# Optimization experiments

Hardware: AMD Instinct MI355X
Metric: run time of the kernel (lower is better)

## Reference

```python
import jax, jax.numpy as jnp
import numpy as np
from jax import lax

B, H, W, Q, C = 2, 96, 96, 30000, 64
DIMS = [C * 9 + 4, 256, 256, 256, 256, 3]  # imnet MLP


def setup_inputs() -> dict:
    key = jax.random.key(0)
    ks = jax.random.split(key, 20)
    d = {}
    d["inp"] = jax.random.normal(ks[0], (B, 3, H, W), jnp.float32)
    d["coord"] = jax.random.uniform(ks[1], (B, Q, 2), jnp.float32) * 2.0 - 1.0
    d["cell"] = jax.random.uniform(ks[2], (B, Q, 2), jnp.float32) * (2.0 / 256.0)
    d["conv_w"] = jax.random.normal(ks[3], (C, 3, 3, 3), jnp.float32) * 0.1
    d["conv_b"] = jnp.zeros((C,), jnp.float32)
    for i in range(5):
        fan_in = DIMS[i]
        d[f"w{i}"] = jax.random.normal(ks[4 + i], (DIMS[i], DIMS[i + 1]), jnp.float32) / np.sqrt(fan_in)
        d[f"b{i}"] = jnp.zeros((DIMS[i + 1],), jnp.float32)
    return d


def _liif_forward(inp, coord, cell, conv_w, conv_b, ws, bs):
    # encoder: 3x3 conv + tanh (gen_feat)
    feat = lax.conv_general_dilated(inp, conv_w, (1, 1), "SAME",
                                    dimension_numbers=("NCHW", "OIHW", "NCHW"))
    feat = jnp.tanh(feat + conv_b[None, :, None, None])  # [B,C,H,W]
    b, c, h, w = feat.shape

    # feat_unfold: F.unfold(feat, 3, padding=1) -> [B, C*9, H, W]
    pad = jnp.pad(feat, ((0, 0), (0, 0), (1, 1), (1, 1)))
    patches = jnp.stack([pad[:, :, i:i + h, j:j + w] for i in range(3) for j in range(3)], axis=2)
    fu = patches.reshape(b, c * 9, h, w).transpose(0, 2, 3, 1)  # [B,H,W,9C]

    # local ensemble offsets
    offsets = jnp.array([[-1., -1.], [-1., 1.], [1., -1.], [1., 1.]], jnp.float32)
    rad = jnp.array([1.0 / h, 1.0 / w], jnp.float32)  # 2/r/2
    eps = 1e-6
    ec = coord[None] + (offsets * rad)[:, None, None, :] + eps  # [4,B,Q,2]
    ec = jnp.clip(ec, -1 + 1e-10, 1 - 1e-10)

    # grid_sample nearest, align_corners=False: ix = ((x+1)*size - 1)/2, round
    iy = jnp.clip(jnp.round((ec[..., 0] + 1) * h / 2 - 0.5).astype(jnp.int32), 0, h - 1)
    ix = jnp.clip(jnp.round((ec[..., 1] + 1) * w / 2 - 0.5).astype(jnp.int32), 0, w - 1)
    b_idx = jnp.arange(b)[None, :, None]  # [1,B,1]
    q_feat = fu[b_idx, iy, ix]  # [4,B,Q,9C]

    # feat_coord (make_coord): pixel-center coords in [-1,1]
    yc = (-1.0 + (2.0 * jnp.arange(h, dtype=jnp.float32) + 1.0) / h)
    xc = (-1.0 + (2.0 * jnp.arange(w, dtype=jnp.float32) + 1.0) / w)
    fc = jnp.stack(jnp.meshgrid(yc, xc, indexing="ij"), axis=-1)  # [H,W,2]
    q_coord = fc[iy, ix]  # [4,B,Q,2]

    scale = jnp.array([h, w], jnp.float32)
    rel_coord = (coord[None] - q_coord) * scale  # [4,B,Q,2]
    rel_cell = cell * scale  # [B,Q,2]

    x = jnp.concatenate(
        [q_feat, rel_coord, jnp.broadcast_to(rel_cell[None], rel_coord.shape)], axis=-1)  # [4,B,Q,580]

    # imnet MLP
    for wi, bi in zip(ws[:-1], bs[:-1]):
        x = jax.nn.relu(x @ wi + bi)
    x = x @ ws[-1] + bs[-1]  # [4,B,Q,3]

    areas = jnp.abs(jnp.prod(rel_coord, axis=-1, keepdims=True)) + 1e-9
    areas = areas / jnp.sum(areas, axis=0, keepdims=True)
    areas = areas[::-1]  # swap diagonal ensemble weights

    out = jnp.sum(x * areas, axis=0)  # [B,Q,3]
    return jnp.tanh(out) * 1.01  # fat_tanh(eps=0.01)


def reference(inp, coord, cell, conv_w, conv_b, w0, b0, w1, b1, w2, b2, w3, b3, w4, b4):
    return _liif_forward(inp, coord, cell, conv_w, conv_b,
                         [w0, w1, w2, w3, w4], [b0, b1, b2, b3, b4])
```

## Files before the change

kernel.cpp:

```cpp
#include <hip/hip_runtime.h>


typedef _Float16 half8   __attribute__((ext_vector_type(8)));
typedef _Float16 half4v  __attribute__((ext_vector_type(4)));
typedef _Float16 half2v  __attribute__((ext_vector_type(2)));
typedef float    float4v __attribute__((ext_vector_type(4)));
typedef float    floatx16 __attribute__((ext_vector_type(16)));

__device__ __forceinline__ _Float16 to_h(float v) {
  return (_Float16)fminf(fmaxf(v, -60000.0f), 60000.0f);
}

#define NQ 30000
#define QT 469
#define QTP 472

__global__ void prep_kernel(const float* __restrict__ w0,
                            const float* __restrict__ w1,
                            const float* __restrict__ w2,
                            const float* __restrict__ w3,
                            const float* __restrict__ w4,
                            _Float16* __restrict__ p0, _Float16* __restrict__ p1,
                            _Float16* __restrict__ p2, _Float16* __restrict__ p3,
                            _Float16* __restrict__ p4) {
  int idx = blockIdx.x * 256 + threadIdx.x;
  if (idx < 151552) {
    int kb = idx >> 11, rem = idx & 2047;
    int n = rem >> 3, i = rem & 7;
    int f = kb * 8 + i;
    float v = 0.0f;
    if (f < 576)      v = w0[((f & 63) * 9 + (f >> 6)) * 256 + n];
    else if (f < 580) v = w0[f * 256 + n];
    p0[idx] = (_Float16)v;
  } else if (idx < 348160) {
    int j = idx - 151552;
    int l = j >> 16;
    int j2 = j & 65535;
    int kb = j2 >> 11, rem = j2 & 2047;
    int n = rem >> 3, i = rem & 7;
    int k = kb * 8 + i;
    const float* w = (l == 0) ? w1 : (l == 1) ? w2 : w3;
    _Float16* p = (l == 0) ? p1 : (l == 1) ? p2 : p3;
    p[j2] = (_Float16)w[k * 256 + n];
  } else if (idx < 352256) {
    int j = idx - 348160;
    int kb = j >> 7, rem = j & 127;
    int n = rem >> 3, i = rem & 7;
    int k = kb * 8 + i;
    float v = (n < 3) ? w4[k * 3 + n] : 0.0f;
    p4[j] = (_Float16)v;
  }
}

__global__ void conv_kernel(const float* __restrict__ inp,
                            const float* __restrict__ cw,
                            const float* __restrict__ cb,
                            _Float16* __restrict__ P) {
  __shared__ __align__(16) float s_w[1728];
  __shared__ __align__(16) float s_b[64];
  for (int i = threadIdx.x; i < 1728; i += 256) s_w[i] = cw[i];
  if (threadIdx.x < 64) s_b[threadIdx.x] = cb[threadIdx.x];
  __syncthreads();
  int tid = blockIdx.x * 256 + threadIdx.x;
  if (tid >= 2 * 98 * 98) return;
  int b = tid / 9604;
  int rem = tid % 9604;
  int yy = rem / 98, xx = rem % 98;
  alignas(16) _Float16 outv[64];
  if (yy == 0 || yy == 97 || xx == 0 || xx == 97) {
#pragma unroll
    for (int c = 0; c < 64; ++c) outv[c] = (_Float16)0.0f;
  } else {
    int y = yy - 1, x = xx - 1;
    float win[27];
#pragma unroll
    for (int ci = 0; ci < 3; ++ci)
#pragma unroll
      for (int ky = 0; ky < 3; ++ky)
#pragma unroll
        for (int kx = 0; kx < 3; ++kx) {
          int yi = y + ky - 1, xi = x + kx - 1;
          float v = 0.0f;
          if (yi >= 0 && yi < 96 && xi >= 0 && xi < 96)
            v = inp[((b * 3 + ci) * 96 + yi) * 96 + xi];
          win[ci * 9 + ky * 3 + kx] = v;
        }
    for (int co = 0; co < 64; ++co) {
      float acc = s_b[co];
#pragma unroll
      for (int k = 0; k < 27; ++k) acc = fmaf(win[k], s_w[co * 27 + k], acc);
      outv[co] = (_Float16)tanhf(acc);
    }
  }
  _Float16* dst = P + tid * 64;
#pragma unroll
  for (int j = 0; j < 8; ++j) ((half8*)dst)[j] = ((const half8*)outv)[j];
}

__global__ __launch_bounds__(256, 2) void gmat_kernel(
    const _Float16* __restrict__ P,
    const _Float16* __restrict__ wp0,
    _Float16* __restrict__ G) {
  const int t    = threadIdx.x;
  const int lane = t & 63;
  const int wv   = t >> 6;
  const int ln32 = lane & 31;
  const int hi   = lane >> 5;
  const int pb   = blockIdx.x * 128;

  int voffB[4]; int gidx[4];
#pragma unroll
  for (int nt2 = 0; nt2 < 4; ++nt2) {
    int g   = pb + nt2 * 32 + ln32;
    int bb  = g / 9216;
    int rem = g - bb * 9216;
    int ry  = rem / 96;
    int rx  = rem - ry * 96;
    int pix = (bb * 98 + ry) * 98 + rx;
    voffB[nt2] = pix * 128 + hi * 16;
    gidx[nt2]  = pix * 256;
  }
  const char* Pb = (const char*)P;
  const _Float16* wb0 = wp0 + (hi * 256 + wv * 64 + ln32) * 8;

  floatx16 acc[2][4];
#pragma unroll
  for (int mt2 = 0; mt2 < 2; ++mt2)
#pragma unroll
    for (int nt2 = 0; nt2 < 4; ++nt2) acc[mt2][nt2] = (floatx16)(0.0f);

  half8 bfA[4], bfB[4], afA[2], afB[2];
  afA[0] = *(const half8*)(wb0);          afA[1] = *(const half8*)(wb0 + 256);
  afB[0] = *(const half8*)(wb0 + 4096);   afB[1] = *(const half8*)(wb0 + 4096 + 256);
#pragma unroll
  for (int nt2 = 0; nt2 < 4; ++nt2) {
    bfA[nt2] = *(const half8*)(Pb + voffB[nt2]);
    bfB[nt2] = *(const half8*)(Pb + voffB[nt2] + 32);
  }
#pragma unroll 1
  for (int s = 0; s < 36; s += 2) {
#pragma unroll
    for (int mt2 = 0; mt2 < 2; ++mt2)
#pragma unroll
      for (int nt2 = 0; nt2 < 4; ++nt2)
        acc[mt2][nt2] = __builtin_amdgcn_mfma_f32_32x32x16_f16(
            afA[mt2], bfA[nt2], acc[mt2][nt2], 0, 0, 0);
    {
      const int sp = (s + 2 <= 35) ? (s + 2) : 35;
      const int patch = sp >> 2;
      const int off = ((patch / 3) * 98 + (patch % 3)) * 128 + ((sp & 3) << 5);
      afA[0] = *(const half8*)(wb0 + sp * 4096);
      afA[1] = *(const half8*)(wb0 + sp * 4096 + 256);
#pragma unroll
      for (int nt2 = 0; nt2 < 4; ++nt2)
        bfA[nt2] = *(const half8*)(Pb + voffB[nt2] + off);
    }
#pragma unroll
    for (int mt2 = 0; mt2 < 2; ++mt2)
#pragma unroll
      for (int nt2 = 0; nt2 < 4; ++nt2)
        acc[mt2][nt2] = __builtin_amdgcn_mfma_f32_32x32x16_f16(
            afB[mt2], bfB[nt2], acc[mt2][nt2], 0, 0, 0);
    {
      const int sp = (s + 3 <= 35) ? (s + 3) : 35;
      const int patch = sp >> 2;
      const int off = ((patch / 3) * 98 + (patch % 3)) * 128 + ((sp & 3) << 5);
      afB[0] = *(const half8*)(wb0 + sp * 4096);
      afB[1] = *(const half8*)(wb0 + sp * 4096 + 256);
#pragma unroll
      for (int nt2 = 0; nt2 < 4; ++nt2)
        bfB[nt2] = *(const half8*)(Pb + voffB[nt2] + off);
    }
  }
#pragma unroll
  for (int mt2 = 0; mt2 < 2; ++mt2)
#pragma unroll
    for (int nt2 = 0; nt2 < 4; ++nt2) {
      half8 c0, c1;
#pragma unroll
      for (int j = 0; j < 8; ++j) {
        c0[j] = (_Float16)acc[mt2][nt2][j];
        c1[j] = (_Float16)acc[mt2][nt2][8 + j];
      }
      _Float16* ga = G + gidx[nt2] + (wv * 2 + mt2) * 32 + hi * 16;
      *(half8*)(ga)     = c0;
      *(half8*)(ga + 8) = c1;
    }
}

__device__ __forceinline__ void writeback32(floatx16 (&acc)[2][4],
                                            const float* __restrict__ sb,
                                            _Float16 (*s_h)[264],
                                            int wv, int ln32, int hi) {
#pragma unroll
  for (int mt2 = 0; mt2 < 2; ++mt2) {
    const int mb = wv * 64 + mt2 * 32 + 4 * hi;
#pragma unroll
    for (int g = 0; g < 4; ++g) {
      const int m0 = mb + 8 * g;
      float b0 = sb[m0], b1 = sb[m0 + 1], b2 = sb[m0 + 2], b3 = sb[m0 + 3];
#pragma unroll
      for (int nt2 = 0; nt2 < 4; ++nt2) {
        const int n = nt2 * 32 + ln32;
        float v0 = fmaxf(acc[mt2][nt2][4 * g + 0] + b0, 0.0f);
        float v1 = fmaxf(acc[mt2][nt2][4 * g + 1] + b1, 0.0f);
        float v2 = fmaxf(acc[mt2][nt2][4 * g + 2] + b2, 0.0f);
        float v3 = fmaxf(acc[mt2][nt2][4 * g + 3] + b3, 0.0f);
        half2v lo  = __builtin_bit_cast(half2v, __builtin_amdgcn_cvt_pkrtz(v0, v1));
        half2v hi2 = __builtin_bit_cast(half2v, __builtin_amdgcn_cvt_pkrtz(v2, v3));
        half4v hv;
        hv[0] = lo[0]; hv[1] = lo[1]; hv[2] = hi2[0]; hv[3] = hi2[1];
        *(half4v*)(&s_h[n][m0]) = hv;
      }
    }
  }
}

__device__ __forceinline__ void layer256(const _Float16* __restrict__ wbl,
                                         _Float16 (*s_h)[264],
                                         int ln32, int hi,
                                         floatx16 (&acc)[2][4]) {
#pragma unroll
  for (int mt2 = 0; mt2 < 2; ++mt2)
#pragma unroll
    for (int nt2 = 0; nt2 < 4; ++nt2) acc[mt2][nt2] = (floatx16)(0.0f);
  half8 afA[2], afB[2], bfA[4], bfB[4];
  afA[0] = *(const half8*)(wbl);
  afA[1] = *(const half8*)(wbl + 256);
  afB[0] = *(const half8*)(wbl + 4096);
  afB[1] = *(const half8*)(wbl + 4096 + 256);
#pragma unroll
  for (int nt2 = 0; nt2 < 4; ++nt2) {
    bfA[nt2] = *(const half8*)(&s_h[nt2 * 32 + ln32][hi * 8]);
    bfB[nt2] = *(const half8*)(&s_h[nt2 * 32 + ln32][16 + hi * 8]);
  }
#pragma unroll 1
  for (int s = 0; s < 16; s += 2) {
#pragma unroll
    for (int mt2 = 0; mt2 < 2; ++mt2)
#pragma unroll
      for (int nt2 = 0; nt2 < 4; ++nt2)
        acc[mt2][nt2] = __builtin_amdgcn_mfma_f32_32x32x16_f16(
            afA[mt2], bfA[nt2], acc[mt2][nt2], 0, 0, 0);
    {
      const int sc = (s + 2 < 16) ? (s + 2) : 0;
      const int sw = (s + 2 < 16) ? (s + 2) : 15;
      afA[0] = *(const half8*)(wbl + sw * 4096);
      afA[1] = *(const half8*)(wbl + sw * 4096 + 256);
#pragma unroll
      for (int nt2 = 0; nt2 < 4; ++nt2)
        bfA[nt2] = *(const half8*)(&s_h[nt2 * 32 + ln32][sc * 16 + hi * 8]);
    }
#pragma unroll
    for (int mt2 = 0; mt2 < 2; ++mt2)
#pragma unroll
      for (int nt2 = 0; nt2 < 4; ++nt2)
        acc[mt2][nt2] = __builtin_amdgcn_mfma_f32_32x32x16_f16(
            afB[mt2], bfB[nt2], acc[mt2][nt2], 0, 0, 0);
    {
      const int sc = (s + 3 < 16) ? (s + 3) : 0;
      const int sw = (s + 3 < 16) ? (s + 3) : 15;
      afB[0] = *(const half8*)(wbl + sw * 4096);
      afB[1] = *(const half8*)(wbl + sw * 4096 + 256);
#pragma unroll
      for (int nt2 = 0; nt2 < 4; ++nt2)
        bfB[nt2] = *(const half8*)(&s_h[nt2 * 32 + ln32][sc * 16 + hi * 8]);
    }
  }
}

__global__ __launch_bounds__(256, 2) void liif_main(
    const float* __restrict__ coord, const float* __restrict__ cell,
    const float* __restrict__ bias0, const float* __restrict__ bias1,
    const float* __restrict__ bias2, const float* __restrict__ bias3,
    const float* __restrict__ bias4,
    const _Float16* __restrict__ G,
    const _Float16* __restrict__ wp0, const _Float16* __restrict__ wp1,
    const _Float16* __restrict__ wp2, const _Float16* __restrict__ wp3,
    const _Float16* __restrict__ wp4,
    float* __restrict__ out) {
  __shared__ __align__(16) int      s_pix[4][64];
  __shared__ __align__(16) float    s_area[4][64];
  __shared__ __align__(16) _Float16 s_ext[4][64][8];
  __shared__ __align__(16) float    s_bias[1028];
  __shared__ __align__(16) float    s_out[128][4];
  __shared__ __align__(16) float    s_num[64][4];
  __shared__ __align__(16) _Float16 s_h[128][264];

  const int t   = threadIdx.x;
  const int blk = blockIdx.x;
  const int bb  = (blk & 4) >> 2;
  const int tile = (blk >> 3) * 4 + (blk & 3);
  const int q0  = tile * 64;

  for (int i = t; i < 1027; i += 256) {
    float v;
    if (i < 256)       v = bias0[i];
    else if (i < 512)  v = bias1[i - 256];
    else if (i < 768)  v = bias2[i - 512];
    else if (i < 1024) v = bias3[i - 768];
    else               v = bias4[i - 1024];
    s_bias[i] = v;
  }

  if (t < 64) {
    int q = q0 + t;
    bool valid = q < NQ;
    float c0 = 0.f, c1 = 0.f, e0 = 0.f, e1 = 0.f;
    if (valid) {
      int base = (bb * NQ + q) * 2;
      c0 = coord[base]; c1 = coord[base + 1];
      e0 = cell[base];  e1 = cell[base + 1];
    }
    float rc0 = e0 * 96.0f, rc1 = e1 * 96.0f;
#pragma unroll
    for (int o = 0; o < 4; ++o) {
      float oy = (o < 2) ? -1.0f : 1.0f;
      float ox = (o & 1) ? 1.0f : -1.0f;
      float ec0 = (c0 + oy * (1.0f / 96.0f)) + 1e-6f;
      float ec1 = (c1 + ox * (1.0f / 96.0f)) + 1e-6f;
      ec0 = fminf(fmaxf(ec0, -1.0f), 1.0f);
      ec1 = fminf(fmaxf(ec1, -1.0f), 1.0f);
      int iy = (int)rintf(((ec0 + 1.0f) * 96.0f) * 0.5f - 0.5f);
      int ix = (int)rintf(((ec1 + 1.0f) * 96.0f) * 0.5f - 0.5f);
      iy = min(max(iy, 0), 95); ix = min(max(ix, 0), 95);
      float qc0 = -1.0f + (2.0f * (float)iy + 1.0f) / 96.0f;
      float qc1 = -1.0f + (2.0f * (float)ix + 1.0f) / 96.0f;
      float r0 = (c0 - qc0) * 96.0f;
      float r1 = (c1 - qc1) * 96.0f;
      s_pix[o][t]  = (bb * 98 + iy) * 98 + ix;
      s_area[o][t] = fabsf(r0 * r1) + 1e-9f;
      s_ext[o][t][0] = to_h(r0);  s_ext[o][t][1] = to_h(r1);
      s_ext[o][t][2] = to_h(rc0); s_ext[o][t][3] = to_h(rc1);
      s_ext[o][t][4] = (_Float16)0.0f; s_ext[o][t][5] = (_Float16)0.0f;
      s_ext[o][t][6] = (_Float16)0.0f; s_ext[o][t][7] = (_Float16)0.0f;
    }
    s_num[t][0] = 0.f; s_num[t][1] = 0.f; s_num[t][2] = 0.f; s_num[t][3] = 0.f;
  }
  __syncthreads();

  const int lane = t & 63;
  const int wv   = t >> 6;
  const int ln32 = lane & 31;
  const int hi   = lane >> 5;
  const int ln16 = lane & 15;
  const int lg   = lane >> 4;

  const _Float16* wb0 = wp0 + (hi * 256 + wv * 64 + ln32) * 8;
  const _Float16* wb1 = wp1 + (hi * 256 + wv * 64 + ln32) * 8;
  const _Float16* wb2 = wp2 + (hi * 256 + wv * 64 + ln32) * 8;
  const _Float16* wb3 = wp3 + (hi * 256 + wv * 64 + ln32) * 8;

#pragma unroll 1
  for (int p = 0; p < 2; ++p) {
    int pixr[4]; int eidx[4];
#pragma unroll
    for (int nt2 = 0; nt2 < 4; ++nt2) {
      int r = nt2 * 32 + ln32;
      int o = p * 2 + (r >> 6);
      int q = r & 63;
      pixr[nt2] = s_pix[o][q];
      eidx[nt2] = (o * 64 + q) * 8;
    }

    floatx16 acc[2][4];
#pragma unroll
    for (int mt2 = 0; mt2 < 2; ++mt2)
#pragma unroll
      for (int nt2 = 0; nt2 < 4; ++nt2) {
        const _Float16* ga = G + pixr[nt2] * 256 + (wv * 2 + mt2) * 32 + hi * 16;
        half8 g0 = *(const half8*)(ga);
        half8 g1 = *(const half8*)(ga + 8);
        floatx16 a;
#pragma unroll
        for (int j = 0; j < 8; ++j) {
          a[j]     = (float)g0[j];
          a[8 + j] = (float)g1[j];
        }
        acc[mt2][nt2] = a;
      }
    {
      half8 ae[2];
      ae[0] = *(const half8*)(wb0 + 36 * 4096);
      ae[1] = *(const half8*)(wb0 + 36 * 4096 + 256);
      half8 z = {(_Float16)0, (_Float16)0, (_Float16)0, (_Float16)0,
                 (_Float16)0, (_Float16)0, (_Float16)0, (_Float16)0};
      half8 bfe[4];
#pragma unroll
      for (int nt2 = 0; nt2 < 4; ++nt2)
        bfe[nt2] = (hi == 0) ? *(const half8*)(&s_ext[0][0][0] + eidx[nt2]) : z;
#pragma unroll
      for (int mt2 = 0; mt2 < 2; ++mt2)
#pragma unroll
        for (int nt2 = 0; nt2 < 4; ++nt2)
          acc[mt2][nt2] = __builtin_amdgcn_mfma_f32_32x32x16_f16(
              ae[mt2], bfe[nt2], acc[mt2][nt2], 0, 0, 0);
    }
    writeback32(acc, s_bias, s_h, wv, ln32, hi);
    __syncthreads();

    layer256(wb1, s_h, ln32, hi, acc);
    __syncthreads();
    writeback32(acc, s_bias + 256, s_h, wv, ln32, hi);
    __syncthreads();

    layer256(wb2, s_h, ln32, hi, acc);
    __syncthreads();
    writeback32(acc, s_bias + 512, s_h, wv, ln32, hi);
    __syncthreads();

    layer256(wb3, s_h, ln32, hi, acc);
    __syncthreads();
    writeback32(acc, s_bias + 768, s_h, wv, ln32, hi);
    __syncthreads();

    half8 af4 = *(const half8*)(wp4 + (lg * 16 + ln16) * 8);
    float4v a4[2];
    a4[0] = (float4v){0.f, 0.f, 0.f, 0.f};
    a4[1] = (float4v){0.f, 0.f, 0.f, 0.f};
#pragma unroll 1
    for (int s = 0; s < 8; ++s) {
      half8 afc = af4;
      if (s < 7)
        af4 = *(const half8*)(wp4 + (((s + 1) * 4 + lg) * 16 + ln16) * 8);
#pragma unroll
      for (int u = 0; u < 2; ++u) {
        int row = (2 * wv + u) * 16 + ln16;
        half8 bf = *(const half8*)(&s_h[row][s * 32 + lg * 8]);
        a4[u] = __builtin_amdgcn_mfma_f32_16x16x32_f16(afc, bf, a4[u], 0, 0, 0);
      }
    }
    if (lg == 0) {
#pragma unroll
      for (int u = 0; u < 2; ++u) {
        int row = (2 * wv + u) * 16 + ln16;
        *(float4v*)(&s_out[row][0]) = a4[u];
      }
    }
    __syncthreads();

    if (t < 64) {
      float a_lo = s_area[3 - 2 * p][t];
      float a_hi = s_area[2 - 2 * p][t];
#pragma unroll
      for (int j = 0; j < 3; ++j)
        s_num[t][j] += s_out[t][j] * a_lo + s_out[64 + t][j] * a_hi;
    }
  }

  if (t < 64) {
    int q = q0 + t;
    if (q < NQ) {
      float den = s_area[0][t] + s_area[1][t] + s_area[2][t] + s_area[3][t];
      int ob = (bb * NQ + q) * 3;
#pragma unroll
      for (int j = 0; j < 3; ++j) {
        float v = s_num[t][j] / den + s_bias[1024 + j];
        out[ob + j] = tanhf(v) * 1.01f;
      }
    }
  }
}

extern "C" void kernel_launch(void* const* d_in, const int* in_sizes, int n_in,
                              void* d_out, int out_size, void* d_ws, size_t ws_size,
                              hipStream_t stream) {
  const float* inp   = (const float*)d_in[0];
  const float* coord = (const float*)d_in[1];
  const float* cell  = (const float*)d_in[2];
  const float* cw    = (const float*)d_in[3];
  const float* cb    = (const float*)d_in[4];
  const float* w0    = (const float*)d_in[5];
  const float* b0    = (const float*)d_in[6];
  const float* w1    = (const float*)d_in[7];
  const float* b1    = (const float*)d_in[8];
  const float* w2    = (const float*)d_in[9];
  const float* b2    = (const float*)d_in[10];
  const float* w3    = (const float*)d_in[11];
  const float* b3    = (const float*)d_in[12];
  const float* w4    = (const float*)d_in[13];
  const float* b4    = (const float*)d_in[14];

  char* ws = (char*)d_ws;
  _Float16* P   = (_Float16*)(ws);
  _Float16* wp0 = (_Float16*)(ws + 2458624);
  _Float16* wp1 = (_Float16*)(ws + 2761728);
  _Float16* wp2 = (_Float16*)(ws + 2892800);
  _Float16* wp3 = (_Float16*)(ws + 3023872);
  _Float16* wp4 = (_Float16*)(ws + 3154944);
  _Float16* G   = (_Float16*)(ws + 3163136);
  float* outp = (float*)d_out;

  hipLaunchKernelGGL(prep_kernel, dim3(1376), dim3(256), 0, stream,
                     w0, w1, w2, w3, w4, wp0, wp1, wp2, wp3, wp4);
  hipLaunchKernelGGL(conv_kernel, dim3(76), dim3(256), 0, stream, inp, cw, cb, P);
  hipLaunchKernelGGL(gmat_kernel, dim3(144), dim3(256), 0, stream, P, wp0, G);
  hipLaunchKernelGGL(liif_main, dim3(8 * (QTP / 4)), dim3(256), 0, stream,
                     coord, cell, b0, b1, b2, b3, b4,
                     G, wp0, wp1, wp2, wp3, wp4, outp);
}
```

Measured before the change: 269.2 us.

## Merge weight prep with conv launch and halve gmat tile for more blocks

The weight-packing and conv encoder kernels are merged into one launch, with block ranges dispatched by blockIdx, which removes one kernel launch and its serialization gap. The gmat kernel tile is halved from 128 to 64 pixels per block, doubling the grid from 144 to 288 blocks so more CUs are busy. Its K loop is also restructured into a three-stage register prefetch. Each block now re-reads the weight fragments for fewer pixels, which increases weight traffic.

```diff
diff --git a/kernel.cpp b/kernel.cpp
--- a/kernel.cpp
+++ b/kernel.cpp
@@ -15,53 +15,54 @@
 #define QT 469
 #define QTP 472
 
-__global__ void prep_kernel(const float* __restrict__ w0,
-                            const float* __restrict__ w1,
-                            const float* __restrict__ w2,
-                            const float* __restrict__ w3,
-                            const float* __restrict__ w4,
-                            _Float16* __restrict__ p0, _Float16* __restrict__ p1,
-                            _Float16* __restrict__ p2, _Float16* __restrict__ p3,
-                            _Float16* __restrict__ p4) {
-  int idx = blockIdx.x * 256 + threadIdx.x;
-  if (idx < 151552) {
-    int kb = idx >> 11, rem = idx & 2047;
-    int n = rem >> 3, i = rem & 7;
-    int f = kb * 8 + i;
-    float v = 0.0f;
-    if (f < 576)      v = w0[((f & 63) * 9 + (f >> 6)) * 256 + n];
-    else if (f < 580) v = w0[f * 256 + n];
-    p0[idx] = (_Float16)v;
-  } else if (idx < 348160) {
-    int j = idx - 151552;
-    int l = j >> 16;
-    int j2 = j & 65535;
-    int kb = j2 >> 11, rem = j2 & 2047;
-    int n = rem >> 3, i = rem & 7;
-    int k = kb * 8 + i;
-    const float* w = (l == 0) ? w1 : (l == 1) ? w2 : w3;
-    _Float16* p = (l == 0) ? p1 : (l == 1) ? p2 : p3;
-    p[j2] = (_Float16)w[k * 256 + n];
-  } else if (idx < 352256) {
-    int j = idx - 348160;
-    int kb = j >> 7, rem = j & 127;
-    int n = rem >> 3, i = rem & 7;
-    int k = kb * 8 + i;
-    float v = (n < 3) ? w4[k * 3 + n] : 0.0f;
-    p4[j] = (_Float16)v;
-  }
-}
-
-__global__ void conv_kernel(const float* __restrict__ inp,
-                            const float* __restrict__ cw,
-                            const float* __restrict__ cb,
-                            _Float16* __restrict__ P) {
+__global__ void prep_conv_kernel(const float* __restrict__ w0,
+                                 const float* __restrict__ w1,
+                                 const float* __restrict__ w2,
+                                 const float* __restrict__ w3,
+                                 const float* __restrict__ w4,
+                                 const float* __restrict__ inp,
+                                 const float* __restrict__ cw,
+                                 const float* __restrict__ cb,
+                                 _Float16* __restrict__ p0, _Float16* __restrict__ p1,
+                                 _Float16* __restrict__ p2, _Float16* __restrict__ p3,
+                                 _Float16* __restrict__ p4,
+                                 _Float16* __restrict__ P) {
   __shared__ __align__(16) float s_w[1728];
   __shared__ __align__(16) float s_b[64];
+  if (blockIdx.x < 1376) {
+    int idx = blockIdx.x * 256 + threadIdx.x;
+    if (idx < 151552) {
+      int kb = idx >> 11, rem = idx & 2047;
+      int n = rem >> 3, i = rem & 7;
+      int f = kb * 8 + i;
+      float v = 0.0f;
+      if (f < 576)      v = w0[((f & 63) * 9 + (f >> 6)) * 256 + n];
+      else if (f < 580) v = w0[f * 256 + n];
+      p0[idx] = (_Float16)v;
+    } else if (idx < 348160) {
+      int j = idx - 151552;
+      int l = j >> 16;
+      int j2 = j & 65535;
+      int kb = j2 >> 11, rem = j2 & 2047;
+      int n = rem >> 3, i = rem & 7;
+      int k = kb * 8 + i;
+      const float* w = (l == 0) ? w1 : (l == 1) ? w2 : w3;
+      _Float16* p = (l == 0) ? p1 : (l == 1) ? p2 : p3;
+      p[j2] = (_Float16)w[k * 256 + n];
+    } else if (idx < 352256) {
+      int j = idx - 348160;
+      int kb = j >> 7, rem = j & 127;
+      int n = rem >> 3, i = rem & 7;
+      int k = kb * 8 + i;
+      float v = (n < 3) ? w4[k * 3 + n] : 0.0f;
+      p4[j] = (_Float16)v;
+    }
+    return;
+  }
   for (int i = threadIdx.x; i < 1728; i += 256) s_w[i] = cw[i];
   if (threadIdx.x < 64) s_b[threadIdx.x] = cb[threadIdx.x];
   __syncthreads();
-  int tid = blockIdx.x * 256 + threadIdx.x;
+  int tid = (blockIdx.x - 1376) * 256 + threadIdx.x;
   if (tid >= 2 * 98 * 98) return;
   int b = tid / 9604;
   int rem = tid % 9604;
@@ -106,11 +107,11 @@
   const int wv   = t >> 6;
   const int ln32 = lane & 31;
   const int hi   = lane >> 5;
-  const int pb   = blockIdx.x * 128;
-
-  int voffB[4]; int gidx[4];
-#pragma unroll
-  for (int nt2 = 0; nt2 < 4; ++nt2) {
+  const int pb   = blockIdx.x * 64;
+
+  int voffB[2]; int gidx[2];
+#pragma unroll
+  for (int nt2 = 0; nt2 < 2; ++nt2) {
     int g   = pb + nt2 * 32 + ln32;
     int bb  = g / 9216;
     int rem = g - bb * 9216;
@@ -123,59 +124,78 @@
   const char* Pb = (const char*)P;
   const _Float16* wb0 = wp0 + (hi * 256 + wv * 64 + ln32) * 8;
 
-  floatx16 acc[2][4];
+  floatx16 acc[2][2];
 #pragma unroll
   for (int mt2 = 0; mt2 < 2; ++mt2)
 #pragma unroll
-    for (int nt2 = 0; nt2 < 4; ++nt2) acc[mt2][nt2] = (floatx16)(0.0f);
-
-  half8 bfA[4], bfB[4], afA[2], afB[2];
-  afA[0] = *(const half8*)(wb0);          afA[1] = *(const half8*)(wb0 + 256);
-  afB[0] = *(const half8*)(wb0 + 4096);   afB[1] = *(const half8*)(wb0 + 4096 + 256);
-#pragma unroll
-  for (int nt2 = 0; nt2 < 4; ++nt2) {
+    for (int nt2 = 0; nt2 < 2; ++nt2) acc[mt2][nt2] = (floatx16)(0.0f);
+
+  half8 bfA[2], bfB[2], bfC[2], afA[2], afB[2], afC[2];
+#pragma unroll
+  for (int nt2 = 0; nt2 < 2; ++nt2) {
     bfA[nt2] = *(const half8*)(Pb + voffB[nt2]);
     bfB[nt2] = *(const half8*)(Pb + voffB[nt2] + 32);
-  }
+    bfC[nt2] = *(const half8*)(Pb + voffB[nt2] + 64);
+  }
+  afA[0] = *(const half8*)(wb0);            afA[1] = *(const half8*)(wb0 + 256);
+  afB[0] = *(const half8*)(wb0 + 4096);     afB[1] = *(const half8*)(wb0 + 4096 + 256);
+  afC[0] = *(const half8*)(wb0 + 8192);     afC[1] = *(const half8*)(wb0 + 8192 + 256);
+
 #pragma unroll 1
-  for (int s = 0; s < 36; s += 2) {
+  for (int s = 0; s < 36; s += 3) {
 #pragma unroll
     for (int mt2 = 0; mt2 < 2; ++mt2)
 #pragma unroll
-      for (int nt2 = 0; nt2 < 4; ++nt2)
+      for (int nt2 = 0; nt2 < 2; ++nt2)
         acc[mt2][nt2] = __builtin_amdgcn_mfma_f32_32x32x16_f16(
             afA[mt2], bfA[nt2], acc[mt2][nt2], 0, 0, 0);
     {
-      const int sp = (s + 2 <= 35) ? (s + 2) : 35;
+      const int sp = (s + 3 <= 35) ? (s + 3) : 35;
       const int patch = sp >> 2;
       const int off = ((patch / 3) * 98 + (patch % 3)) * 128 + ((sp & 3) << 5);
       afA[0] = *(const half8*)(wb0 + sp * 4096);
       afA[1] = *(const half8*)(wb0 + sp * 4096 + 256);
 #pragma unroll
-      for (int nt2 = 0; nt2 < 4; ++nt2)
+      for (int nt2 = 0; nt2 < 2; ++nt2)
         bfA[nt2] = *(const half8*)(Pb + voffB[nt2] + off);
     }
 #pragma unroll
     for (int mt2 = 0; mt2 < 2; ++mt2)
 #pragma unroll
-      for (int nt2 = 0; nt2 < 4; ++nt2)
+      for (int nt2 = 0; nt2 < 2; ++nt2)
         acc[mt2][nt2] = __builtin_amdgcn_mfma_f32_32x32x16_f16(
             afB[mt2], bfB[nt2], acc[mt2][nt2], 0, 0, 0);
     {
-      const int sp = (s + 3 <= 35) ? (s + 3) : 35;
+      const int sp = (s + 4 <= 35) ? (s + 4) : 35;
       const int patch = sp >> 2;
       const int off = ((patch / 3) * 98 + (patch % 3)) * 128 + ((sp & 3) << 5);
       afB[0] = *(const half8*)(wb0 + sp * 4096);
       afB[1] = *(const half8*)(wb0 + sp * 4096 + 256);
 #pragma unroll
-      for (int nt2 = 0; nt2 < 4; ++nt2)
+      for (int nt2 = 0; nt2 < 2; ++nt2)
         bfB[nt2] = *(const half8*)(Pb + voffB[nt2] + off);
     }
+#pragma unroll
+    for (int mt2 = 0; mt2 < 2; ++mt2)
+#pragma unroll
+      for (int nt2 = 0; nt2 < 2; ++nt2)
+        acc[mt2][nt2] = __builtin_amdgcn_mfma_f32_32x32x16_f16(
+            afC[mt2], bfC[nt2], acc[mt2][nt2], 0, 0, 0);
+    {
+      const int sp = (s + 5 <= 35) ? (s + 5) : 35;
+      const int patch = sp >> 2;
+      const int off = ((patch / 3) * 98 + (patch % 3)) * 128 + ((sp & 3) << 5);
+      afC[0] = *(const half8*)(wb0 + sp * 4096);
+      afC[1] = *(const half8*)(wb0 + sp * 4096 + 256);
+#pragma unroll
+      for (int nt2 = 0; nt2 < 2; ++nt2)
+        bfC[nt2] = *(const half8*)(Pb + voffB[nt2] + off);
+    }
   }
 #pragma unroll
   for (int mt2 = 0; mt2 < 2; ++mt2)
 #pragma unroll
-    for (int nt2 = 0; nt2 < 4; ++nt2) {
+    for (int nt2 = 0; nt2 < 2; ++nt2) {
       half8 c0, c1;
 #pragma unroll
       for (int j = 0; j < 8; ++j) {
@@ -491,10 +511,10 @@
   _Float16* G   = (_Float16*)(ws + 3163136);
   float* outp = (float*)d_out;
 
-  hipLaunchKernelGGL(prep_kernel, dim3(1376), dim3(256), 0, stream,
-                     w0, w1, w2, w3, w4, wp0, wp1, wp2, wp3, wp4);
-  hipLaunchKernelGGL(conv_kernel, dim3(76), dim3(256), 0, stream, inp, cw, cb, P);
-  hipLaunchKernelGGL(gmat_kernel, dim3(144), dim3(256), 0, stream, P, wp0, G);
+  hipLaunchKernelGGL(prep_conv_kernel, dim3(1452), dim3(256), 0, stream,
+                     w0, w1, w2, w3, w4, inp, cw, cb,
+                     wp0, wp1, wp2, wp3, wp4, P);
+  hipLaunchKernelGGL(gmat_kernel, dim3(288), dim3(256), 0, stream, P, wp0, G);
   hipLaunchKernelGGL(liif_main, dim3(8 * (QTP / 4)), dim3(256), 0, stream,
                      coord, cell, b0, b1, b2, b3, b4,
                      G, wp0, wp1, wp2, wp3, wp4, outp);
```

Measured after the change: 284.1 us. +5.5%, slower.
